# Kernel optimization log

Measured on AMD Instinct MI355X. Metric: run time of the kernel, lower is better.

## Reference

```python
import jax, jax.numpy as jnp
import numpy as np

N = 50000        # num nodes (num_paths)
E = 1_600_000    # num edges (avg degree 32)
W = 64           # window_size -> x feature dim
H = 128          # hidden_dimension
TEMP = 1.0       # temperature


def setup_inputs() -> dict:
    key = jax.random.key(0)
    k = jax.random.split(key, 6)
    x = jax.random.normal(k[0], (N, W), dtype=jnp.float32)
    y = jax.random.normal(k[1], (N,), dtype=jnp.float32)
    edge_index = jax.random.randint(k[2], (2, E), 0, N, dtype=jnp.int32)
    w1 = jax.random.normal(k[3], (2 * W, H), dtype=jnp.float32) / np.sqrt(2 * W)
    b1 = jnp.zeros((H,), dtype=jnp.float32)
    w2 = jax.random.normal(k[4], (H, 1), dtype=jnp.float32) / np.sqrt(H)
    b2 = jnp.zeros((1,), dtype=jnp.float32)
    return {"x": x, "y": y, "edge_index": edge_index,
            "w1": w1, "b1": b1, "w2": w2, "b2": b2}


def reference(x, y, edge_index, w1, b1, w2, b2):
    src, dst = edge_index[0], edge_index[1]
    # edge-wise gather + concat: [E, 2W]
    feat = jnp.concatenate([x[src], x[dst]], axis=1)
    # attention MLP: Linear -> ReLU -> Linear
    h = jax.nn.relu(feat @ w1 + b1)          # [E, H]
    logits = (h @ w2 + b2)[:, 0] / TEMP      # [E]
    # segment softmax over destination nodes (numerically stable)
    m = jax.ops.segment_max(logits, dst, num_segments=N)      # [N]
    e = jnp.exp(logits - m[dst])                               # [E]
    denom = jax.ops.segment_sum(e, dst, num_segments=N)       # [N]
    alpha = e / denom[dst]                                     # [E]
    # weighted scatter-sum aggregation
    y_hat = jax.ops.segment_sum(y[src] * alpha, dst, num_segments=N)  # [N]
    return y_hat, alpha[:, None]
```

## Files before the change

### kernel.cpp

```cpp
#include <hip/hip_runtime.h>
#include <hip/hip_bf16.h>

__device__ __forceinline__ unsigned short f2bf(float f) {
    unsigned u = __float_as_uint(f);
    unsigned r = (u + 0x7fffu + ((u >> 16) & 1u)) >> 16;
    return (unsigned short)r;
}
__device__ __forceinline__ float bfu(unsigned short s) {
    return __uint_as_float(((unsigned)s) << 16);
}
__device__ __forceinline__ float blo(unsigned u) { return __uint_as_float(u << 16); }
__device__ __forceinline__ float bhi(unsigned u) { return __uint_as_float(u & 0xffff0000u); }

__device__ __forceinline__ float dot8_relu(const uint4 a, const uint4 b, const float* w2r) {
    float acc;
    acc  = w2r[0] * fmaxf(blo(a.x) + blo(b.x), 0.f);
    acc += w2r[1] * fmaxf(bhi(a.x) + bhi(b.x), 0.f);
    acc += w2r[2] * fmaxf(blo(a.y) + blo(b.y), 0.f);
    acc += w2r[3] * fmaxf(bhi(a.y) + bhi(b.y), 0.f);
    acc += w2r[4] * fmaxf(blo(a.z) + blo(b.z), 0.f);
    acc += w2r[5] * fmaxf(bhi(a.z) + bhi(b.z), 0.f);
    acc += w2r[6] * fmaxf(blo(a.w) + blo(b.w), 0.f);
    acc += w2r[7] * fmaxf(bhi(a.w) + bhi(b.w), 0.f);
    return acc;
}

__global__ __launch_bounds__(256) void proj_kernel(
    const float* __restrict__ x, const float* __restrict__ w1, const float* __restrict__ b1,
    unsigned short* __restrict__ P, int N)
{
    __shared__ unsigned short wl[64 * 256];
    __shared__ float xs[32 * 64];
    const int t = threadIdx.x;

    for (int i = t; i < 64 * 256; i += 256) {
        int k = i >> 8, j = i & 255;
        float w = (j < 128) ? w1[k * 128 + j] : w1[(64 + k) * 128 + (j - 128)];
        wl[i] = f2bf(w);
    }
    const int n0 = blockIdx.x * 32;
    for (int i = t; i < 32 * 64; i += 256) {
        int n = n0 + (i >> 6);
        xs[i] = (n < N) ? x[(size_t)n * 64 + (i & 63)] : 0.f;
    }
    __syncthreads();

    const int jg = t & 63;
    const int ng = t >> 6;
    const int j0 = jg * 4;

    float acc[8][4];
#pragma unroll
    for (int i = 0; i < 8; ++i)
#pragma unroll
        for (int c = 0; c < 4; ++c) acc[i][c] = 0.f;

    for (int k = 0; k < 64; k += 4) {
        float wv[4][4];
#pragma unroll
        for (int kk = 0; kk < 4; ++kk) {
            ushort4 wu = *(const ushort4*)&wl[(k + kk) * 256 + j0];
            wv[kk][0] = bfu(wu.x); wv[kk][1] = bfu(wu.y);
            wv[kk][2] = bfu(wu.z); wv[kk][3] = bfu(wu.w);
        }
#pragma unroll
        for (int i = 0; i < 8; ++i) {
            const float4 xv = *(const float4*)&xs[(ng * 8 + i) * 64 + k];
#pragma unroll
            for (int c = 0; c < 4; ++c)
                acc[i][c] += xv.x * wv[0][c] + xv.y * wv[1][c] + xv.z * wv[2][c] + xv.w * wv[3][c];
        }
    }

    float bb[4] = {0.f, 0.f, 0.f, 0.f};
    if (j0 < 128) {
#pragma unroll
        for (int c = 0; c < 4; ++c) bb[c] = b1[j0 + c];
    }

#pragma unroll
    for (int i = 0; i < 8; ++i) {
        int n = n0 + ng * 8 + i;
        if (n < N) {
            ushort4 st;
            st.x = f2bf(acc[i][0] + bb[0]);
            st.y = f2bf(acc[i][1] + bb[1]);
            st.z = f2bf(acc[i][2] + bb[2]);
            st.w = f2bf(acc[i][3] + bb[3]);
            *(ushort4*)(P + (size_t)n * 256 + j0) = st;
        }
    }
}

__global__ __launch_bounds__(256) void edge_logit_kernel(
    const unsigned short* __restrict__ P, const int* __restrict__ ei,
    const float* __restrict__ y,
    const float* __restrict__ w2, const float* __restrict__ b2,
    float* __restrict__ elog, unsigned long long* __restrict__ agg, int E)
{
    const int lane = threadIdx.x & 15;
    float w2r[8];
#pragma unroll
    for (int c = 0; c < 8; ++c) w2r[c] = w2[lane * 8 + c];
    const float b2s = b2[0];

    const int slot = (blockIdx.x * 256 + threadIdx.x) >> 4;
    const int nslots = (gridDim.x * 256) >> 4;

    for (int e = slot; e < E; e += nslots) {
        const int s = ei[e];
        const int d = ei[E + e];
        const uint4 a = *(const uint4*)(P + (size_t)s * 256 + lane * 8);
        const uint4 b = *(const uint4*)(P + (size_t)d * 256 + 128 + lane * 8);

        float acc = dot8_relu(a, b, w2r);
        acc += __shfl_xor(acc, 1);
        acc += __shfl_xor(acc, 2);
        acc += __shfl_xor(acc, 4);
        acc += __shfl_xor(acc, 8);

        if (lane == 0) {
            float ev = __expf(acc + b2s);
            elog[e] = ev;
            float flo = fminf(ev * 65536.f, 1.0e9f);
            float fhi = fmaxf(fminf(y[s] * ev * 16384.f, 1.0e9f), -1.0e9f);
            unsigned int qlo = (unsigned int)__float2int_rn(flo);
            int          qhi = __float2int_rn(fhi);
            unsigned long long packed =
                ((unsigned long long)(unsigned int)qhi << 32) | (unsigned long long)qlo;
            atomicAdd(&agg[d], packed);
        }
    }
}

__global__ void node_decode_kernel(const unsigned long long* __restrict__ agg,
                                   float* __restrict__ inv_d,
                                   float* __restrict__ yhat, int N) {
    int i = blockIdx.x * 256 + threadIdx.x;
    if (i >= N) return;
    unsigned long long v = agg[i];
    unsigned int lo = (unsigned int)(v & 0xffffffffull);
    int          hi = (int)(v >> 32);
    if (lo != 0u) {
        float flo = (float)lo;
        yhat[i]  = 4.0f * (float)hi / flo;
        inv_d[i] = 65536.0f / flo;
    } else {
        yhat[i]  = 0.f;
        inv_d[i] = 0.f;
    }
}

__global__ __launch_bounds__(256) void alpha_norm_kernel(
    const int* __restrict__ ei, float* __restrict__ elog,
    const float* __restrict__ inv_d, int E)
{
    int e = blockIdx.x * 256 + threadIdx.x;
    if (e >= E) return;
    int d = ei[E + e];
    elog[e] = elog[e] * inv_d[d];
}

extern "C" void kernel_launch(void* const* d_in, const int* in_sizes, int n_in,
                              void* d_out, int out_size, void* d_ws, size_t ws_size,
                              hipStream_t stream) {
    const float* x  = (const float*)d_in[0];
    const float* y  = (const float*)d_in[1];
    const int*   ei = (const int*)d_in[2];
    const float* w1 = (const float*)d_in[3];
    const float* b1 = (const float*)d_in[4];
    const float* w2 = (const float*)d_in[5];
    const float* b2 = (const float*)d_in[6];

    const int N = in_sizes[1];
    const int E = in_sizes[2] / 2;

    float* out  = (float*)d_out;
    float* yhat = out;
    float* elog = out + N;

    char* ws = (char*)d_ws;
    unsigned short* P = (unsigned short*)ws;
    size_t Pbytes = (size_t)N * 256 * sizeof(unsigned short);
    unsigned long long* agg = (unsigned long long*)(ws + Pbytes);
    float* inv_d = (float*)(ws + Pbytes + (size_t)N * 8);

    hipMemsetAsync(agg, 0, (size_t)N * 8, stream);
    proj_kernel<<<(N + 31) / 32, 256, 0, stream>>>(x, w1, b1, P, N);
    edge_logit_kernel<<<2048, 256, 0, stream>>>(P, ei, y, w2, b2, elog, agg, E);
    node_decode_kernel<<<(N + 255) / 256, 256, 0, stream>>>(agg, inv_d, yhat, N);
    alpha_norm_kernel<<<(E + 255) / 256, 256, 0, stream>>>(ei, elog, inv_d, E);
}
```

Before: 242.0 us.

## Fold agg zeroing into projection, merge decode and normalize kernels, enlarge proj tile

Removes the hipMemsetAsync by zeroing the aggregation buffer inside the projection kernel. It also fuses node decode and alpha normalization into one tail kernel that recomputes the inverse denominator from agg per edge instead of reading an inv_d buffer. The projection kernel now processes 64 nodes per block with 16 rows per thread, which halves the number of weight-table conversions into LDS. This cuts launch overhead and intermediate traffic, at the cost of more registers and a per-edge divide on a 64-bit gather.

```diff
diff --git a/kernel.cpp b/kernel.cpp
--- a/kernel.cpp
+++ b/kernel.cpp
@@ -27,19 +27,24 @@
 
 __global__ __launch_bounds__(256) void proj_kernel(
     const float* __restrict__ x, const float* __restrict__ w1, const float* __restrict__ b1,
-    unsigned short* __restrict__ P, int N)
+    unsigned short* __restrict__ P, unsigned long long* __restrict__ agg, int N)
 {
     __shared__ unsigned short wl[64 * 256];
-    __shared__ float xs[32 * 64];
+    __shared__ float xs[64 * 64];
     const int t = threadIdx.x;
+    const int n0 = blockIdx.x * 64;
+
+    if (t < 64) {
+        int n = n0 + t;
+        if (n < N) agg[n] = 0ull;
+    }
 
     for (int i = t; i < 64 * 256; i += 256) {
         int k = i >> 8, j = i & 255;
         float w = (j < 128) ? w1[k * 128 + j] : w1[(64 + k) * 128 + (j - 128)];
         wl[i] = f2bf(w);
     }
-    const int n0 = blockIdx.x * 32;
-    for (int i = t; i < 32 * 64; i += 256) {
+    for (int i = t; i < 64 * 64; i += 256) {
         int n = n0 + (i >> 6);
         xs[i] = (n < N) ? x[(size_t)n * 64 + (i & 63)] : 0.f;
     }
@@ -49,26 +54,26 @@
     const int ng = t >> 6;
     const int j0 = jg * 4;
 
-    float acc[8][4];
+    float acc[16][4];
 #pragma unroll
-    for (int i = 0; i < 8; ++i)
+    for (int i = 0; i < 16; ++i)
 #pragma unroll
         for (int c = 0; c < 4; ++c) acc[i][c] = 0.f;
 
-    for (int k = 0; k < 64; k += 4) {
-        float wv[4][4];
+    for (int k = 0; k < 64; k += 2) {
+        float wv[2][4];
 #pragma unroll
-        for (int kk = 0; kk < 4; ++kk) {
+        for (int kk = 0; kk < 2; ++kk) {
             ushort4 wu = *(const ushort4*)&wl[(k + kk) * 256 + j0];
             wv[kk][0] = bfu(wu.x); wv[kk][1] = bfu(wu.y);
             wv[kk][2] = bfu(wu.z); wv[kk][3] = bfu(wu.w);
         }
 #pragma unroll
-        for (int i = 0; i < 8; ++i) {
-            const float4 xv = *(const float4*)&xs[(ng * 8 + i) * 64 + k];
+        for (int i = 0; i < 16; ++i) {
+            const float2 xv = *(const float2*)&xs[(ng * 16 + i) * 64 + k];
 #pragma unroll
             for (int c = 0; c < 4; ++c)
-                acc[i][c] += xv.x * wv[0][c] + xv.y * wv[1][c] + xv.z * wv[2][c] + xv.w * wv[3][c];
+                acc[i][c] += xv.x * wv[0][c] + xv.y * wv[1][c];
         }
     }
 
@@ -79,8 +84,8 @@
     }
 
 #pragma unroll
-    for (int i = 0; i < 8; ++i) {
-        int n = n0 + ng * 8 + i;
+    for (int i = 0; i < 16; ++i) {
+        int n = n0 + ng * 16 + i;
         if (n < N) {
             ushort4 st;
             st.x = f2bf(acc[i][0] + bb[0]);
@@ -133,32 +138,25 @@
     }
 }
 
-__global__ void node_decode_kernel(const unsigned long long* __restrict__ agg,
-                                   float* __restrict__ inv_d,
-                                   float* __restrict__ yhat, int N) {
-    int i = blockIdx.x * 256 + threadIdx.x;
-    if (i >= N) return;
-    unsigned long long v = agg[i];
-    unsigned int lo = (unsigned int)(v & 0xffffffffull);
-    int          hi = (int)(v >> 32);
-    if (lo != 0u) {
-        float flo = (float)lo;
-        yhat[i]  = 4.0f * (float)hi / flo;
-        inv_d[i] = 65536.0f / flo;
-    } else {
-        yhat[i]  = 0.f;
-        inv_d[i] = 0.f;
+__global__ __launch_bounds__(256) void tail_kernel(
+    const int* __restrict__ ei, const unsigned long long* __restrict__ agg,
+    float* __restrict__ elog, float* __restrict__ yhat, int N, int E)
+{
+    const int idx = blockIdx.x * 256 + threadIdx.x;
+
+    if (idx < N) {
+        unsigned long long v = agg[idx];
+        unsigned int lo = (unsigned int)(v & 0xffffffffull);
+        int          hi = (int)(v >> 32);
+        yhat[idx] = (lo != 0u) ? 4.0f * (float)hi / (float)lo : 0.f;
     }
-}
 
-__global__ __launch_bounds__(256) void alpha_norm_kernel(
-    const int* __restrict__ ei, float* __restrict__ elog,
-    const float* __restrict__ inv_d, int E)
-{
-    int e = blockIdx.x * 256 + threadIdx.x;
-    if (e >= E) return;
-    int d = ei[E + e];
-    elog[e] = elog[e] * inv_d[d];
+    if (idx < E) {
+        const int d = ei[E + idx];
+        unsigned int lo = (unsigned int)(agg[d] & 0xffffffffull);
+        const float inv = (lo != 0u) ? 65536.0f / (float)lo : 0.f;
+        elog[idx] = elog[idx] * inv;
+    }
 }
 
 extern "C" void kernel_launch(void* const* d_in, const int* in_sizes, int n_in,
@@ -183,11 +181,8 @@
     unsigned short* P = (unsigned short*)ws;
     size_t Pbytes = (size_t)N * 256 * sizeof(unsigned short);
     unsigned long long* agg = (unsigned long long*)(ws + Pbytes);
-    float* inv_d = (float*)(ws + Pbytes + (size_t)N * 8);
 
-    hipMemsetAsync(agg, 0, (size_t)N * 8, stream);
-    proj_kernel<<<(N + 31) / 32, 256, 0, stream>>>(x, w1, b1, P, N);
+    proj_kernel<<<(N + 63) / 64, 256, 0, stream>>>(x, w1, b1, P, agg, N);
     edge_logit_kernel<<<2048, 256, 0, stream>>>(P, ei, y, w2, b2, elog, agg, E);
-    node_decode_kernel<<<(N + 255) / 256, 256, 0, stream>>>(agg, inv_d, yhat, N);
-    alpha_norm_kernel<<<(E + 255) / 256, 256, 0, stream>>>(ei, elog, inv_d, E);
+    tail_kernel<<<(E + 255) / 256, 256, 0, stream>>>(ei, agg, elog, yhat, N, E);
 }
```

Result: slower. 249.2 us (median of 2 runs) (+3.0%).
